# Kernel tuning notes

Measured on AMD Instinct MI355X. Metric: run time of the kernel, lower is better.

## Reference

```python
import jax, jax.numpy as jnp
import numpy as np

B, L, E, H, DV, V = 256, 512, 200, 256, 30000, 50000
NEG_INF = -jnp.inf

def setup_inputs() -> dict:
    key = jax.random.key(0)
    ks = jax.random.split(key, 16)
    s = 0.05
    f = jnp.float32
    return {
        "input_id": jax.random.randint(ks[0], (B, 1), 0, V),
        "input_emb": jax.random.normal(ks[1], (B, 1, E), f),
        "encoder_outputs": jax.random.normal(ks[2], (B, L, H), f),
        "encoder_input_ids": jax.random.randint(ks[3], (B, L), 0, V),
        "hidden": jax.random.normal(ks[4], (B, 1, H), f),
        "attention": jax.random.normal(ks[5], (B, 1, H), f),
        # GRU (PyTorch layout): W_ih (3H, 2H+E), W_hh (3H, H), gate order r,z,n
        "W_ih": jax.random.normal(ks[6], (3 * H, 2 * H + E), f) * s,
        "W_hh": jax.random.normal(ks[7], (3 * H, H), f) * s,
        "b_ih": jnp.zeros((3 * H,), f),
        "b_hh": jnp.zeros((3 * H,), f),
        "W_attn": jax.random.normal(ks[8], (H, H), f) * s,
        "b_attn": jnp.zeros((H,), f),
        "W_comb": jax.random.normal(ks[9], (H, 2 * H), f) * s,
        "b_comb": jnp.zeros((H,), f),
        "W_gen": jax.random.normal(ks[10], (DV, H), f) * s,
        "b_gen": jnp.zeros((DV,), f),
        "W_copy": jax.random.normal(ks[11], (H, H), f) * s,
        "b_copy": jnp.zeros((H,), f),
    }


def reference(input_id, input_emb, encoder_outputs, encoder_input_ids, hidden,
              attention, W_ih, W_hh, b_ih, b_hh, W_attn, b_attn, W_comb,
              b_comb, W_gen, b_gen, W_copy, b_copy):
    b, l = encoder_input_ids.shape
    # selective read: rou = normalized match mask (NaN guard -> 0)
    mask = (input_id == encoder_input_ids).astype(encoder_outputs.dtype)  # (b,l)
    msum = jnp.sum(mask, axis=1, keepdims=True)
    rou = jnp.where(msum > 0, mask / jnp.where(msum > 0, msum, 1.0), 0.0)
    selective_read = jnp.einsum('bl,blh->bh', rou, encoder_outputs)  # (b,h)

    # GRU single step (dropout is identity at inference)
    x = jnp.concatenate([input_emb[:, 0], attention[:, 0], selective_read], axis=-1)
    h_prev = hidden[:, 0]  # (b,h)
    gx = x @ W_ih.T + b_ih          # (b,3h)
    gh = h_prev @ W_hh.T + b_hh     # (b,3h)
    xr, xz, xn = jnp.split(gx, 3, axis=-1)
    hr, hz, hn = jnp.split(gh, 3, axis=-1)
    r = jax.nn.sigmoid(xr + hr)
    z = jax.nn.sigmoid(xz + hz)
    n = jnp.tanh(xn + r * hn)
    h = (1.0 - z) * n + z * h_prev  # (b,h) cur_hidden

    # attention
    q = h @ W_attn.T + b_attn
    attn_w = jax.nn.softmax(jnp.einsum('bh,blh->bl', q, encoder_outputs), axis=-1)
    attn_applied = jnp.einsum('bl,blh->bh', attn_w, encoder_outputs)
    cur_attention = jnp.tanh(
        jnp.concatenate([attn_applied, h], axis=-1) @ W_comb.T + b_comb)  # (b,h)

    # generate + copy scores, joint softmax
    generate_score = cur_attention @ W_gen.T + b_gen                     # (b,DV)
    copy_weights = jax.nn.sigmoid(encoder_outputs @ W_copy.T + b_copy)   # (b,l,h)
    copy_score = jnp.einsum('blh,bh->bl', copy_weights, cur_attention)   # (b,l)
    score = jax.nn.softmax(jnp.concatenate([generate_score, copy_score], axis=1), axis=1)
    gen_s, copy_s = score[:, :DV], score[:, DV:]

    # fused equivalent of the one-hot scatter/mix: direct scatter-add into vocab
    output = jnp.zeros((b, V), score.dtype)
    output = output.at[:, :DV].add(gen_s)
    output = output.at[jnp.arange(b)[:, None], encoder_input_ids].add(copy_s)

    pos = output > 0
    out = jnp.where(pos, jnp.log(jnp.where(pos, output, 1.0)), NEG_INF)
    return out, h[:, None, :], cur_attention[:, None, :]
```

## Files before the change

kernel.cpp:

```cpp
#include <hip/hip_runtime.h>
#include <cmath>

#define B_  256
#define L_  512
#define E_  200
#define H_  256
#define DV_ 30000
#define V_  50000
#define X_  712
#define G3_ 768
#define NT_ 235
#define NBC_ 1024
#define NBG_ 470

#define NEG_BIG -1.0e30f

typedef __attribute__((ext_vector_type(8))) _Float16 half8;
typedef __attribute__((ext_vector_type(4))) float   floatx4;

#define GLOAD16(gptr, lptr)                                                            \
    __builtin_amdgcn_global_load_lds(                                                  \
        (const __attribute__((address_space(1))) unsigned int*)(gptr),                 \
        (__attribute__((address_space(3))) unsigned int*)(lptr), 16, 0, 0)

__global__ void k_selread(const int* __restrict__ input_id, const float* __restrict__ emb,
                          const float* __restrict__ attention, const float* __restrict__ hidden,
                          const float* __restrict__ enc, const int* __restrict__ enc_ids,
                          const float* __restrict__ Wc, _Float16* __restrict__ wcb,
                          float* __restrict__ xT) {
    int b = blockIdx.x, t = threadIdx.x;
    __shared__ int cnt;
    __shared__ int list[L_];
    if (t == 0) cnt = 0;
    __syncthreads();
    wcb[b * H_ + t] = (_Float16)Wc[b * H_ + t];
    int id = input_id[b];
    for (int l = t; l < L_; l += 256) {
        if (enc_ids[b * L_ + l] == id) { int p = atomicAdd(&cnt, 1); list[p] = l; }
    }
    __syncthreads();
    int n = cnt;
    float s = 0.f;
    for (int i = 0; i < n; i++) s += enc[(b * L_ + list[i]) * H_ + t];
    float sel = (n > 0) ? s / (float)n : 0.f;
    for (int k = t; k < E_; k += 256) xT[k * B_ + b] = emb[b * E_ + k];
    xT[(E_ + t) * B_ + b]       = attention[b * H_ + t];
    xT[(E_ + H_ + t) * B_ + b]  = sel;
    xT[(X_ + t) * B_ + b]       = hidden[b * H_ + t];
}

template<int K, int OS>
__global__ void __launch_bounds__(256) k_gru_one(const float* __restrict__ xTp, const float* __restrict__ W,
                                                 const float* __restrict__ bias, float* __restrict__ g) {
    __shared__ __align__(16) float Ws[8 * K];
    int t  = threadIdx.x;
    int j0 = blockIdx.x * 8;
    int bq = t & 63;
    int jh = t >> 6;
#pragma unroll
    for (int jj = 0; jj < 8; jj++) {
        const float4* src = (const float4*)(W + (size_t)(j0 + jj) * K);
        float4* dst = (float4*)(Ws + jj * K);
        for (int i = t; i < K / 4; i += 256) dst[i] = src[i];
    }
    __syncthreads();
    float acc0[4] = {0.f, 0.f, 0.f, 0.f};
    float acc1[4] = {0.f, 0.f, 0.f, 0.f};
    const float* w0 = Ws + (jh * 2 + 0) * K;
    const float* w1 = Ws + (jh * 2 + 1) * K;
#pragma unroll 2
    for (int k4 = 0; k4 < K / 4; k4++) {
        float4 wa = *(const float4*)(w0 + k4 * 4);
        float4 wb = *(const float4*)(w1 + k4 * 4);
        float wav[4] = {wa.x, wa.y, wa.z, wa.w};
        float wbv[4] = {wb.x, wb.y, wb.z, wb.w};
#pragma unroll
        for (int u = 0; u < 4; u++) {
            float4 xv = *(const float4*)(xTp + (size_t)(k4 * 4 + u) * B_ + bq * 4);
            acc0[0] += wav[u] * xv.x; acc0[1] += wav[u] * xv.y;
            acc0[2] += wav[u] * xv.z; acc0[3] += wav[u] * xv.w;
            acc1[0] += wbv[u] * xv.x; acc1[1] += wbv[u] * xv.y;
            acc1[2] += wbv[u] * xv.z; acc1[3] += wbv[u] * xv.w;
        }
    }
    int ja = j0 + jh * 2, jb = ja + 1;
    float ba = bias[ja], bb = bias[jb];
#pragma unroll
    for (int i = 0; i < 4; i++) {
        g[(size_t)(bq * 4 + i) * OS + ja] = acc0[i] + ba;
        g[(size_t)(bq * 4 + i) * OS + jb] = acc1[i] + bb;
    }
}

__global__ void k_gru_gates(const float* __restrict__ gx, const float* __restrict__ gh,
                            const float* __restrict__ hidden, float* __restrict__ hws,
                            float* __restrict__ hT, float* __restrict__ hout) {
    int b = blockIdx.x, j = threadIdx.x;
    float xr = gx[b * G3_ + j], xz = gx[b * G3_ + 256 + j], xn = gx[b * G3_ + 512 + j];
    float hr = gh[b * G3_ + j], hz = gh[b * G3_ + 256 + j], hn = gh[b * G3_ + 512 + j];
    float r = 1.f / (1.f + expf(-(xr + hr)));
    float z = 1.f / (1.f + expf(-(xz + hz)));
    float n = tanhf(xn + r * hn);
    float hp = hidden[b * H_ + j];
    float h = (1.f - z) * n + z * hp;
    hws[b * H_ + j] = h;
    hT[j * B_ + b]  = h;
    hout[b * H_ + j] = h;
}

#define NC_ 4
#define CR_ 128
__global__ void __launch_bounds__(256) k_attn_a(const float* __restrict__ qws, const float* __restrict__ enc,
                         float* __restrict__ avp, float* __restrict__ mdp) {
    int blk = blockIdx.x;
    int b = blk >> 2, c = blk & 3;
    int t = threadIdx.x, lane = t & 63, w = t >> 6;
    __shared__ float ps[CR_];
    __shared__ float red[8];
    __shared__ __align__(16) float pavs[4][H_];
    const float* encc = enc + ((size_t)b * L_ + c * CR_) * H_;
    float4 q4 = *(const float4*)&qws[b * H_ + lane * 4];
    for (int i = 0; i < 32; i += 8) {
        float s[8];
#pragma unroll
        for (int u = 0; u < 8; u++) {
            float4 e = *(const float4*)(encc + (size_t)(w * 32 + i + u) * H_ + lane * 4);
            s[u] = q4.x * e.x + q4.y * e.y + q4.z * e.z + q4.w * e.w;
        }
#pragma unroll
        for (int u = 0; u < 8; u++) {
#pragma unroll
            for (int o = 1; o < 64; o <<= 1) s[u] += __shfl_xor(s[u], o);
            if (lane == 0) ps[w * 32 + i + u] = s[u];
        }
    }
    __syncthreads();
    {
        float v = ps[w * 32 + (lane & 31)];
#pragma unroll
        for (int o = 1; o < 64; o <<= 1) v = fmaxf(v, __shfl_xor(v, o));
        if (lane == 0) red[w] = v;
    }
    __syncthreads();
    float M = fmaxf(fmaxf(red[0], red[1]), fmaxf(red[2], red[3]));
    float e = (t < CR_) ? __expf(ps[t] - M) : 0.f;
    {
        float ssum = e;
#pragma unroll
        for (int o = 1; o < 64; o <<= 1) ssum += __shfl_xor(ssum, o);
        if (lane == 0) red[4 + w] = ssum;
    }
    __syncthreads();
    if (t < CR_) ps[t] = e;
    if (t == 0) {
        mdp[blk * 2]     = M;
        mdp[blk * 2 + 1] = red[4] + red[5] + red[6] + red[7];
    }
    __syncthreads();
    {
        float4 av = {0.f, 0.f, 0.f, 0.f};
        const float* encg = encc + (size_t)w * 32 * H_;
        const float* psg  = &ps[w * 32];
#pragma unroll 4
        for (int r = 0; r < 32; r++) {
            float p = psg[r];
            float4 ev = *(const float4*)(encg + (size_t)r * H_ + lane * 4);
            av.x += p * ev.x; av.y += p * ev.y; av.z += p * ev.z; av.w += p * ev.w;
        }
        *(float4*)&pavs[w][lane * 4] = av;
    }
    __syncthreads();
    avp[(size_t)blk * H_ + t] = pavs[0][t] + pavs[1][t] + pavs[2][t] + pavs[3][t];
}

__global__ void __launch_bounds__(256) k_attn_b(const float* __restrict__ avp, const float* __restrict__ mdp,
                         const float* __restrict__ hws, const float* __restrict__ W_comb,
                         const float* __restrict__ b_comb,
                         float* __restrict__ caws, _Float16* __restrict__ cab,
                         float* __restrict__ caout) {
    int b = blockIdx.x, t = threadIdx.x;
    __shared__ __align__(16) float xs[2 * H_];
    float m0 = mdp[(b * 4 + 0) * 2], d0 = mdp[(b * 4 + 0) * 2 + 1];
    float m1 = mdp[(b * 4 + 1) * 2], d1 = mdp[(b * 4 + 1) * 2 + 1];
    float m2 = mdp[(b * 4 + 2) * 2], d2 = mdp[(b * 4 + 2) * 2 + 1];
    float m3 = mdp[(b * 4 + 3) * 2], d3 = mdp[(b * 4 + 3) * 2 + 1];
    float M = fmaxf(fmaxf(m0, m1), fmaxf(m2, m3));
    float f0 = __expf(m0 - M), f1 = __expf(m1 - M), f2 = __expf(m2 - M), f3 = __expf(m3 - M);
    float den = f0 * d0 + f1 * d1 + f2 * d2 + f3 * d3;
    float num = f0 * avp[((size_t)b * 4 + 0) * H_ + t] + f1 * avp[((size_t)b * 4 + 1) * H_ + t]
              + f2 * avp[((size_t)b * 4 + 2) * H_ + t] + f3 * avp[((size_t)b * 4 + 3) * H_ + t];
    xs[t]      = num / den;
    xs[H_ + t] = hws[b * H_ + t];
    __syncthreads();
    const float4* wr = (const float4*)(W_comb + (size_t)t * (2 * H_));
    const float4* xp = (const float4*)xs;
    float acc = 0.f;
#pragma unroll 8
    for (int k4 = 0; k4 < 128; k4++) {
        float4 wv = wr[k4], xv = xp[k4];
        acc += wv.x * xv.x + wv.y * xv.y + wv.z * xv.z + wv.w * xv.w;
    }
    float cav = tanhf(b_comb[t] + acc);
    caws[b * H_ + t]  = cav;
    cab[b * H_ + t]   = (_Float16)cav;
    caout[b * H_ + t] = cav;
}

__global__ void __launch_bounds__(256, 2) k_gc(
        const float* __restrict__ enc, const _Float16* __restrict__ wcb,
        const float* __restrict__ b_copy, const float* __restrict__ caws,
        float* __restrict__ copy_s,
        const _Float16* __restrict__ cab, const float* __restrict__ W_gen,
        const float* __restrict__ b_gen, float* __restrict__ out,
        float2* __restrict__ pmd) {
    __shared__ __align__(16) unsigned char smem[67584];
    int t = threadIdx.x, w = t >> 6, lane = t & 63;
    int l15 = lane & 15, q = lane >> 4;

    if (blockIdx.x < NBC_) {
        float*    Af = (float*)smem;
        _Float16* Bh = (_Float16*)(smem + 32768);
        float*    bcs = (float*)(smem + 65536);
        float*    cas = bcs + H_;
        int cb = blockIdx.x;
        int R0 = cb * 128;
        int b  = cb >> 2;
        bcs[t] = b_copy[t];
        cas[t] = caws[b * H_ + t];
        floatx4 acc[2][16];
#pragma unroll
        for (int i = 0; i < 2; i++)
#pragma unroll
            for (int j = 0; j < 16; j++) acc[i][j] = (floatx4){0.f, 0.f, 0.f, 0.f};

#define STAGE_CPY(KC, BUF)                                                              \
        {                                                                               \
            _Pragma("unroll")                                                           \
            for (int i = 0; i < 4; i++) {                                               \
                int t2 = w * 4 + i;                                                     \
                int row = t2 * 8 + (lane >> 3);                                         \
                int sl  = (lane & 7) ^ (row & 7);                                       \
                GLOAD16(enc + (size_t)(R0 + row) * H_ + (KC) + sl * 4,                  \
                        &Af[(BUF) * 4096 + t2 * 256]);                                  \
            }                                                                           \
            _Pragma("unroll")                                                           \
            for (int i = 0; i < 4; i++) {                                               \
                int t2 = w * 4 + i;                                                     \
                int row = t2 * 16 + (lane >> 2);                                        \
                int sl  = (lane & 3) ^ ((row >> 1) & 3);                                \
                GLOAD16(wcb + row * H_ + (KC) + sl * 8,                                 \
                        &Bh[(BUF) * 8192 + t2 * 512]);                                  \
            }                                                                           \
        }
        STAGE_CPY(0, 0);
        __syncthreads();
        int cur = 0;
        for (int kc8 = 0; kc8 < 8; kc8++) {
            if (kc8 < 7) STAGE_CPY((kc8 + 1) * 32, cur ^ 1);
            half8 a[2];
#pragma unroll
            for (int mi = 0; mi < 2; mi++) {
                int m = w * 32 + mi * 16 + l15;
                const float* ar = &Af[cur * 4096 + m * 32];
                float4 f0 = *(const float4*)&ar[((q * 2 + 0) ^ (m & 7)) * 4];
                float4 f1 = *(const float4*)&ar[((q * 2 + 1) ^ (m & 7)) * 4];
                half8 h;
                h[0] = (_Float16)f0.x; h[1] = (_Float16)f0.y; h[2] = (_Float16)f0.z; h[3] = (_Float16)f0.w;
                h[4] = (_Float16)f1.x; h[5] = (_Float16)f1.y; h[6] = (_Float16)f1.z; h[7] = (_Float16)f1.w;
                a[mi] = h;
            }
#pragma unroll
            for (int ni = 0; ni < 16; ni++) {
                int n = ni * 16 + l15;
                half8 bf = *(const half8*)&Bh[cur * 8192 + n * 32 + (q ^ ((n >> 1) & 3)) * 8];
                acc[0][ni] = __builtin_amdgcn_mfma_f32_16x16x32_f16(a[0], bf, acc[0][ni], 0, 0, 0);
                acc[1][ni] = __builtin_amdgcn_mfma_f32_16x16x32_f16(a[1], bf, acc[1][ni], 0, 0, 0);
            }
            __syncthreads();
            cur ^= 1;
        }
#pragma unroll
        for (int mi = 0; mi < 2; mi++) {
#pragma unroll
            for (int j = 0; j < 4; j++) {
                float p = 0.f;
#pragma unroll
                for (int ni = 0; ni < 16; ni++) {
                    int col = ni * 16 + l15;
                    float v = acc[mi][ni][j] + bcs[col];
                    p += cas[col] / (1.f + __expf(-v));
                }
                p += __shfl_xor(p, 1);
                p += __shfl_xor(p, 2);
                p += __shfl_xor(p, 4);
                p += __shfl_xor(p, 8);
                if (l15 == 0) copy_s[R0 + w * 32 + mi * 16 + q * 4 + j] = p;
            }
        }
    } else {
        _Float16* Ah = (_Float16*)smem;
        float*    Bf = (float*)(smem + 16384);
        float*    mm = (float*)(smem + 49152);
        float*    dd = mm + 512;
        int g  = blockIdx.x - NBC_;
        int bx = (g < NT_) ? g : g - NT_;
        int by = (g < NT_) ? 0 : 1;
        int n0 = bx * 128, m0 = by * 128;
        int wm = (w >> 1) * 64, wn = (w & 1) * 64;
        floatx4 acc[4][4];
#pragma unroll
        for (int i = 0; i < 4; i++)
#pragma unroll
            for (int j = 0; j < 4; j++) acc[i][j] = (floatx4){0.f, 0.f, 0.f, 0.f};

#define STAGE_GEN(KC, BUF)                                                              \
        {                                                                               \
            _Pragma("unroll")                                                           \
            for (int i = 0; i < 2; i++) {                                               \
                int t2 = w * 2 + i;                                                     \
                int row = t2 * 16 + (lane >> 2);                                        \
                int sl  = (lane & 3) ^ ((row >> 1) & 3);                                \
                GLOAD16(cab + (size_t)(m0 + row) * H_ + (KC) + sl * 8,                  \
                        &Ah[(BUF) * 4096 + t2 * 512]);                                  \
            }                                                                           \
            _Pragma("unroll")                                                           \
            for (int i = 0; i < 4; i++) {                                               \
                int t2 = w * 4 + i;                                                     \
                int row = t2 * 8 + (lane >> 3);                                         \
                int sl  = (lane & 7) ^ (row & 7);                                       \
                int nn = n0 + row; nn = nn < DV_ ? nn : DV_ - 1;                        \
                GLOAD16(W_gen + (size_t)nn * H_ + (KC) + sl * 4,                        \
                        &Bf[(BUF) * 4096 + t2 * 256]);                                  \
            }                                                                           \
        }
        STAGE_GEN(0, 0);
        __syncthreads();
        int cur = 0;
        for (int kc8 = 0; kc8 < 8; kc8++) {
            if (kc8 < 7) STAGE_GEN((kc8 + 1) * 32, cur ^ 1);
            half8 a[4];
#pragma unroll
            for (int mi = 0; mi < 4; mi++) {
                int m = wm + mi * 16 + l15;
                a[mi] = *(const half8*)&Ah[cur * 4096 + m * 32 + (q ^ ((m >> 1) & 3)) * 8];
            }
#pragma unroll
            for (int ni = 0; ni < 4; ni++) {
                int n = wn + ni * 16 + l15;
                const float* bb = &Bf[cur * 4096 + n * 32];
                float4 f0 = *(const float4*)&bb[((q * 2 + 0) ^ (n & 7)) * 4];
                float4 f1 = *(const float4*)&bb[((q * 2 + 1) ^ (n & 7)) * 4];
                half8 bf;
                bf[0] = (_Float16)f0.x; bf[1] = (_Float16)f0.y; bf[2] = (_Float16)f0.z; bf[3] = (_Float16)f0.w;
                bf[4] = (_Float16)f1.x; bf[5] = (_Float16)f1.y; bf[6] = (_Float16)f1.z; bf[7] = (_Float16)f1.w;
#pragma unroll
                for (int mi = 0; mi < 4; mi++)
                    acc[mi][ni] = __builtin_amdgcn_mfma_f32_16x16x32_f16(a[mi], bf, acc[mi][ni], 0, 0, 0);
            }
            __syncthreads();
            cur ^= 1;
        }
        float bgs[4];
#pragma unroll
        for (int ni = 0; ni < 4; ni++) {
            int col = n0 + wn + ni * 16 + l15;
            if (col < DV_) {
                float bg = b_gen[col];
                bgs[ni] = bg;
#pragma unroll
                for (int mi = 0; mi < 4; mi++)
#pragma unroll
                    for (int j = 0; j < 4; j++) {
                        int row = m0 + wm + mi * 16 + q * 4 + j;
                        out[(size_t)row * V_ + col] = acc[mi][ni][j] + bg;
                    }
            } else bgs[ni] = 0.f;
        }
#pragma unroll
        for (int mi = 0; mi < 4; mi++)
#pragma unroll
            for (int j = 0; j < 4; j++) {
                float m_l = -INFINITY, d_l = 0.f;
#pragma unroll
                for (int ni = 0; ni < 4; ni++) {
                    int col = n0 + wn + ni * 16 + l15;
                    float v = (col < DV_) ? acc[mi][ni][j] + bgs[ni] : NEG_BIG;
                    float mn = fmaxf(m_l, v);
                    d_l = d_l * __expf(m_l - mn) + __expf(v - mn);
                    m_l = mn;
                }
#pragma unroll
                for (int o = 1; o < 16; o <<= 1) {
                    float m2 = __shfl_xor(m_l, o), d2 = __shfl_xor(d_l, o);
                    float mn = fmaxf(m_l, m2);
                    d_l = d_l * __expf(m_l - mn) + d2 * __expf(m2 - mn);
                    m_l = mn;
                }
                if (l15 == 0) {
                    int rl = wm + mi * 16 + q * 4 + j;
                    mm[w * 128 + rl] = m_l; dd[w * 128 + rl] = d_l;
                }
            }
        __syncthreads();
        if (t < 128) {
            int wa = (t < 64) ? 0 : 2;
            float ma = mm[wa * 128 + t],       da = dd[wa * 128 + t];
            float mb = mm[(wa + 1) * 128 + t], db = dd[(wa + 1) * 128 + t];
            float M = fmaxf(ma, mb);
            float D = da * __expf(ma - M) + db * __expf(mb - M);
            pmd[(size_t)(m0 + t) * NT_ + bx] = make_float2(M, D);
        }
    }
}

__global__ void __launch_bounds__(256) k_stats2(const float2* __restrict__ pmd, const float* __restrict__ copy_s,
                         float* __restrict__ mrow, float* __restrict__ ldrow) {
    int b = blockIdx.x, t = threadIdx.x, lane = t & 63, w = t >> 6;
    __shared__ float rm[4], rs[4];
    float m = -INFINITY, d = 0.f;
    if (t < NT_) { float2 p = pmd[(size_t)b * NT_ + t]; m = p.x; d = p.y; }
    float v0 = copy_s[b * L_ + t];
    float v1 = copy_s[b * L_ + 256 + t];
    float mn = fmaxf(m, v0); d = d * __expf(m - mn) + __expf(v0 - mn); m = mn;
    mn = fmaxf(m, v1); d = d * __expf(m - mn) + __expf(v1 - mn); m = mn;
#pragma unroll
    for (int o = 1; o < 64; o <<= 1) {
        float m2 = __shfl_xor(m, o), d2 = __shfl_xor(d, o);
        mn = fmaxf(m, m2);
        d = d * __expf(m - mn) + d2 * __expf(m2 - mn);
        m = mn;
    }
    if (lane == 0) { rm[w] = m; rs[w] = d; }
    __syncthreads();
    if (t == 0) {
        float M = rm[0], S = rs[0];
        for (int i = 1; i < 4; i++) {
            float mx = fmaxf(M, rm[i]);
            S = S * __expf(M - mx) + rs[i] * __expf(rm[i] - mx);
            M = mx;
        }
        mrow[b] = M;
        ldrow[b] = __logf(S);
    }
}

__global__ void __launch_bounds__(256) k_final(float* __restrict__ out, const float* __restrict__ mrow,
                        const float* __restrict__ ldrow) {
    int idx = blockIdx.x * 256 + threadIdx.x;
    int b = blockIdx.y;
    if (idx >= V_ / 4) return;
    float4* o4 = (float4*)(out + (size_t)b * V_) + idx;
    if (idx >= DV_ / 4) {
        *o4 = make_float4(NEG_BIG, NEG_BIG, NEG_BIG, NEG_BIG);
        return;
    }
    float sh = mrow[b] + ldrow[b];
    float4 v = *o4;
    v.x -= sh; v.y -= sh; v.z -= sh; v.w -= sh;
    *o4 = v;
}

__global__ void k_scatter_log(float* __restrict__ out, const float* __restrict__ copy_s,
                              const int* __restrict__ enc_ids, const float* __restrict__ mrow,
                              const float* __restrict__ ldrow) {
    int l = blockIdx.x * 256 + threadIdx.x;
    int b = blockIdx.y;
    float p = __expf(copy_s[b * L_ + l] - mrow[b] - ldrow[b]);
    unsigned int* up = (unsigned int*)(out + (size_t)b * V_ + enc_ids[b * L_ + l]);
    unsigned int cur = *up;
    while (true) {
        float ov = __uint_as_float(cur);
        float pv = (ov < -1.0e29f) ? p : __expf(ov) + p;
        unsigned int prev = atomicCAS(up, cur, __float_as_uint(__logf(pv)));
        if (prev == cur) break;
        cur = prev;
    }
}

extern "C" void kernel_launch(void* const* d_in, const int* in_sizes, int n_in,
                              void* d_out, int out_size, void* d_ws, size_t ws_size,
                              hipStream_t stream) {
    const int*   input_id  = (const int*)  d_in[0];
    const float* input_emb = (const float*)d_in[1];
    const float* enc       = (const float*)d_in[2];
    const int*   enc_ids   = (const int*)  d_in[3];
    const float* hidden    = (const float*)d_in[4];
    const float* attention = (const float*)d_in[5];
    const float* W_ih      = (const float*)d_in[6];
    const float* W_hh      = (const float*)d_in[7];
    const float* b_ih      = (const float*)d_in[8];
    const float* b_hh      = (const float*)d_in[9];
    const float* W_attn    = (const float*)d_in[10];
    const float* b_attn    = (const float*)d_in[11];
    const float* W_comb    = (const float*)d_in[12];
    const float* b_comb    = (const float*)d_in[13];
    const float* W_gen     = (const float*)d_in[14];
    const float* b_gen     = (const float*)d_in[15];
    const float* W_copy    = (const float*)d_in[16];
    const float* b_copy    = (const float*)d_in[17];

    float* out = (float*)d_out;
    float* ws  = (float*)d_ws;
    float* xT   = ws;
    float* gx   = xT + 247808;
    float* gh   = gx + 196608;
    float* hws  = gh + 196608;
    float* caws = hws + 65536;
    float* cps  = caws + 65536;
    float* mrow = cps + 131072;
    float* ldrow = mrow + 256;
    _Float16* wcb = (_Float16*)(ldrow + 256);
    _Float16* cab = wcb + 65536;
    float* qws  = (float*)(cab + 65536);
    float* mdp  = qws + 65536;
    float2* pmd = (float2*)(mdp + 2048);
    float* hT   = xT;
    float* avp  = gx;

    float* hout  = out + (size_t)B_ * V_;
    float* caout = hout + B_ * H_;

    k_selread<<<256, 256, 0, stream>>>(input_id, input_emb, attention, hidden, enc, enc_ids, W_copy, wcb, xT);
    k_gru_one<712, G3_><<<96, 256, 0, stream>>>(xT, W_ih, b_ih, gx);
    k_gru_one<256, G3_><<<96, 256, 0, stream>>>(xT + X_ * B_, W_hh, b_hh, gh);
    k_gru_gates<<<256, 256, 0, stream>>>(gx, gh, hidden, hws, hT, hout);
    k_gru_one<256, H_><<<32, 256, 0, stream>>>(hT, W_attn, b_attn, qws);
    k_attn_a<<<B_ * NC_, 256, 0, stream>>>(qws, enc, avp, mdp);
    k_attn_b<<<256, 256, 0, stream>>>(avp, mdp, hws, W_comb, b_comb, caws, cab, caout);
    k_gc<<<NBC_ + NBG_, 256, 0, stream>>>(enc, wcb, b_copy, caws, cps, cab, W_gen, b_gen, out, pmd);
    k_stats2<<<256, 256, 0, stream>>>(pmd, cps, mrow, ldrow);
    dim3 gf((V_ / 4 + 255) / 256, B_);
    k_final<<<gf, 256, 0, stream>>>(out, mrow, ldrow);
    dim3 gs(L_ / 256, B_);
    k_scatter_log<<<gs, 256, 0, stream>>>(out, cps, enc_ids, mrow, ldrow);
}
```

Before: 444.9 us.

## Prefetch two stages ahead with explicit vmcnt waits in copy and generate GEMMs

Restructures the double-buffered K loops of the copy-score and generate-score MFMA GEMMs. Two stages are issued up front, and each iteration waits with a partial s_waitcnt vmcnt so later global-to-LDS loads stay in flight. The refill of a buffer is issued only after the compute barrier, and sched_barriers pin the ordering. The aim is to hide more global load latency than the old load-next-then-syncthreads scheme. The risk is that hardcoded vmcnt counts must match the number of loads issued per stage, or results will be wrong.

New measurement: 439.9 us. About the same (-1.1%).

```diff
diff --git a/kernel.cpp b/kernel.cpp
--- a/kernel.cpp
+++ b/kernel.cpp
@@ -253,32 +253,40 @@
             }                                                                           \
         }
         STAGE_CPY(0, 0);
+        STAGE_CPY(32, 1);
+#pragma unroll
+        for (int c = 0; c < 8; c++) {
+            if (c < 7) { asm volatile("s_waitcnt vmcnt(8)" ::: "memory"); }
+            else       { asm volatile("s_waitcnt vmcnt(0)" ::: "memory"); }
+            __builtin_amdgcn_s_barrier();
+            __builtin_amdgcn_sched_barrier(0);
+            {
+                half8 a[2];
+#pragma unroll
+                for (int mi = 0; mi < 2; mi++) {
+                    int m = w * 32 + mi * 16 + l15;
+                    const float* ar = &Af[(c & 1) * 4096 + m * 32];
+                    float4 f0 = *(const float4*)&ar[((q * 2 + 0) ^ (m & 7)) * 4];
+                    float4 f1 = *(const float4*)&ar[((q * 2 + 1) ^ (m & 7)) * 4];
+                    half8 h;
+                    h[0] = (_Float16)f0.x; h[1] = (_Float16)f0.y; h[2] = (_Float16)f0.z; h[3] = (_Float16)f0.w;
+                    h[4] = (_Float16)f1.x; h[5] = (_Float16)f1.y; h[6] = (_Float16)f1.z; h[7] = (_Float16)f1.w;
+                    a[mi] = h;
+                }
+#pragma unroll
+                for (int ni = 0; ni < 16; ni++) {
+                    int n = ni * 16 + l15;
+                    half8 bf = *(const half8*)&Bh[(c & 1) * 8192 + n * 32 + (q ^ ((n >> 1) & 3)) * 8];
+                    acc[0][ni] = __builtin_amdgcn_mfma_f32_16x16x32_f16(a[0], bf, acc[0][ni], 0, 0, 0);
+                    acc[1][ni] = __builtin_amdgcn_mfma_f32_16x16x32_f16(a[1], bf, acc[1][ni], 0, 0, 0);
+                }
+            }
+            __builtin_amdgcn_sched_barrier(0);
+            __builtin_amdgcn_s_barrier();
+            __builtin_amdgcn_sched_barrier(0);
+            if (c + 2 < 8) STAGE_CPY((c + 2) * 32, c & 1);
+        }
         __syncthreads();
-        int cur = 0;
-        for (int kc8 = 0; kc8 < 8; kc8++) {
-            if (kc8 < 7) STAGE_CPY((kc8 + 1) * 32, cur ^ 1);
-            half8 a[2];
-#pragma unroll
-            for (int mi = 0; mi < 2; mi++) {
-                int m = w * 32 + mi * 16 + l15;
-                const float* ar = &Af[cur * 4096 + m * 32];
-                float4 f0 = *(const float4*)&ar[((q * 2 + 0) ^ (m & 7)) * 4];
-                float4 f1 = *(const float4*)&ar[((q * 2 + 1) ^ (m & 7)) * 4];
-                half8 h;
-                h[0] = (_Float16)f0.x; h[1] = (_Float16)f0.y; h[2] = (_Float16)f0.z; h[3] = (_Float16)f0.w;
-                h[4] = (_Float16)f1.x; h[5] = (_Float16)f1.y; h[6] = (_Float16)f1.z; h[7] = (_Float16)f1.w;
-                a[mi] = h;
-            }
-#pragma unroll
-            for (int ni = 0; ni < 16; ni++) {
-                int n = ni * 16 + l15;
-                half8 bf = *(const half8*)&Bh[cur * 8192 + n * 32 + (q ^ ((n >> 1) & 3)) * 8];
-                acc[0][ni] = __builtin_amdgcn_mfma_f32_16x16x32_f16(a[0], bf, acc[0][ni], 0, 0, 0);
-                acc[1][ni] = __builtin_amdgcn_mfma_f32_16x16x32_f16(a[1], bf, acc[1][ni], 0, 0, 0);
-            }
-            __syncthreads();
-            cur ^= 1;
-        }
 #pragma unroll
         for (int mi = 0; mi < 2; mi++) {
 #pragma unroll
@@ -334,32 +342,40 @@
             }                                                                           \
         }
         STAGE_GEN(0, 0);
+        STAGE_GEN(32, 1);
+#pragma unroll
+        for (int c = 0; c < 8; c++) {
+            if (c < 7) { asm volatile("s_waitcnt vmcnt(6)" ::: "memory"); }
+            else       { asm volatile("s_waitcnt vmcnt(0)" ::: "memory"); }
+            __builtin_amdgcn_s_barrier();
+            __builtin_amdgcn_sched_barrier(0);
+            {
+                half8 a[4];
+#pragma unroll
+                for (int mi = 0; mi < 4; mi++) {
+                    int m = wm + mi * 16 + l15;
+                    a[mi] = *(const half8*)&Ah[(c & 1) * 4096 + m * 32 + (q ^ ((m >> 1) & 3)) * 8];
+                }
+#pragma unroll
+                for (int ni = 0; ni < 4; ni++) {
+                    int n = wn + ni * 16 + l15;
+                    const float* bb = &Bf[(c & 1) * 4096 + n * 32];
+                    float4 f0 = *(const float4*)&bb[((q * 2 + 0) ^ (n & 7)) * 4];
+                    float4 f1 = *(const float4*)&bb[((q * 2 + 1) ^ (n & 7)) * 4];
+                    half8 bf;
+                    bf[0] = (_Float16)f0.x; bf[1] = (_Float16)f0.y; bf[2] = (_Float16)f0.z; bf[3] = (_Float16)f0.w;
+                    bf[4] = (_Float16)f1.x; bf[5] = (_Float16)f1.y; bf[6] = (_Float16)f1.z; bf[7] = (_Float16)f1.w;
+#pragma unroll
+                    for (int mi = 0; mi < 4; mi++)
+                        acc[mi][ni] = __builtin_amdgcn_mfma_f32_16x16x32_f16(a[mi], bf, acc[mi][ni], 0, 0, 0);
+                }
+            }
+            __builtin_amdgcn_sched_barrier(0);
+            __builtin_amdgcn_s_barrier();
+            __builtin_amdgcn_sched_barrier(0);
+            if (c + 2 < 8) STAGE_GEN((c + 2) * 32, c & 1);
+        }
         __syncthreads();
-        int cur = 0;
-        for (int kc8 = 0; kc8 < 8; kc8++) {
-            if (kc8 < 7) STAGE_GEN((kc8 + 1) * 32, cur ^ 1);
-            half8 a[4];
-#pragma unroll
-            for (int mi = 0; mi < 4; mi++) {
-                int m = wm + mi * 16 + l15;
-                a[mi] = *(const half8*)&Ah[cur * 4096 + m * 32 + (q ^ ((m >> 1) & 3)) * 8];
-            }
-#pragma unroll
-            for (int ni = 0; ni < 4; ni++) {
-                int n = wn + ni * 16 + l15;
-                const float* bb = &Bf[cur * 4096 + n * 32];
-                float4 f0 = *(const float4*)&bb[((q * 2 + 0) ^ (n & 7)) * 4];
-                float4 f1 = *(const float4*)&bb[((q * 2 + 1) ^ (n & 7)) * 4];
-                half8 bf;
-                bf[0] = (_Float16)f0.x; bf[1] = (_Float16)f0.y; bf[2] = (_Float16)f0.z; bf[3] = (_Float16)f0.w;
-                bf[4] = (_Float16)f1.x; bf[5] = (_Float16)f1.y; bf[6] = (_Float16)f1.z; bf[7] = (_Float16)f1.w;
-#pragma unroll
-                for (int mi = 0; mi < 4; mi++)
-                    acc[mi][ni] = __builtin_amdgcn_mfma_f32_16x16x32_f16(a[mi], bf, acc[mi][ni], 0, 0, 0);
-            }
-            __syncthreads();
-            cur ^= 1;
-        }
         float bgs[4];
 #pragma unroll
         for (int ni = 0; ni < 4; ni++) {
```
